# Kernel tuning notes

Measured on AMD Instinct MI355X. Metric: run time of the kernel, lower is better.

Reference implementation:

```python
import jax, jax.numpy as jnp
import numpy as np

N, D, B, K, H, E = 100000, 128, 4096, 64, 256, 128
DIN = D + 1
DELAYED_REWARD_STEP = 100.0


def setup_inputs() -> dict:
    key = jax.random.key(0)
    ks = jax.random.split(key, 16)
    s = 0.02
    d = {}
    d["node_pre_embedding"] = jax.random.normal(ks[0], (N, D), jnp.float32)
    d["steps"] = jax.random.uniform(ks[1], (B,), jnp.float32) * 50.0
    d["h0"] = jax.random.normal(ks[2], (B, H), jnp.float32) * 0.1
    d["c0"] = jax.random.normal(ks[3], (B, H), jnp.float32) * 0.1
    # MLP1: D_in -> 256 -> 128 (action embed, feeds LSTM input)
    d["W1a"] = jax.random.normal(ks[4], (256, DIN), jnp.float32) * s
    d["b1a"] = jnp.zeros((256,), jnp.float32)
    d["W1b"] = jax.random.normal(ks[5], (128, 256), jnp.float32) * s
    d["b1b"] = jnp.zeros((128,), jnp.float32)
    # MLP2: D_in -> 256 -> 128 (neighbor graph embed)
    d["W2a"] = jax.random.normal(ks[6], (256, DIN), jnp.float32) * s
    d["b2a"] = jnp.zeros((256,), jnp.float32)
    d["W2b"] = jax.random.normal(ks[7], (128, 256), jnp.float32) * s
    d["b2b"] = jnp.zeros((128,), jnp.float32)
    # MLP3: lstm_hidden (256) -> 128, single linear (hidden_dims3=[128])
    d["W3"] = jax.random.normal(ks[8], (E, H), jnp.float32) * s
    d["b3"] = jnp.zeros((E,), jnp.float32)
    # LSTMCell (PyTorch layout: gates i,f,g,o stacked on dim 0)
    d["Wih"] = jax.random.normal(ks[9], (4 * H, 128), jnp.float32) * s
    d["Whh"] = jax.random.normal(ks[10], (4 * H, H), jnp.float32) * s
    d["bih"] = jnp.zeros((4 * H,), jnp.float32)
    d["bhh"] = jnp.zeros((4 * H,), jnp.float32)
    # packed ragged adjacency: padded neighbor ids + per-row degree
    d["actions0"] = jax.random.randint(ks[11], (B,), 0, N)
    d["neighbors"] = jax.random.randint(ks[12], (B, K), 0, N)
    d["deg"] = jax.random.randint(ks[13], (B,), 1, K + 1)
    return d


def reference(node_pre_embedding, steps, h0, c0,
              W1a, b1a, W1b, b1b, W2a, b2a, W2b, b2b, W3, b3,
              Wih, Whh, bih, bhh, actions0, neighbors, deg):
    step_scaled = steps / DELAYED_REWARD_STEP  # [B]

    # --- graph embeddings for padded neighbors (ragged gather + MLP2) ---
    nei_feat = node_pre_embedding[neighbors]  # [B, K, D]
    step_col = jnp.broadcast_to(step_scaled[:, None, None], (B, K, 1))
    pre = jnp.concatenate([nei_feat, step_col], axis=-1)  # [B, K, D_in]
    g = jax.nn.relu(jnp.einsum('bkd,hd->bkh', pre, W2a) + b2a)
    g = jnp.einsum('bkh,eh->bke', g, W2b) + b2b  # [B, K, E]

    # --- action embedding: MLP1 -> LSTMCell -> MLP3 ---
    a_pre = jnp.concatenate([node_pre_embedding[actions0], step_scaled[:, None]], axis=-1)
    x = jax.nn.relu(a_pre @ W1a.T + b1a) @ W1b.T + b1b  # [B, 128]
    gates = x @ Wih.T + bih + h0 @ Whh.T + bhh  # [B, 4H]
    i, f, gg, o = jnp.split(gates, 4, axis=-1)
    c = jax.nn.sigmoid(f) * c0 + jax.nn.sigmoid(i) * jnp.tanh(gg)
    h = jax.nn.sigmoid(o) * jnp.tanh(c)
    emb = h @ W3.T + b3  # [B, E]

    # --- scaled dot-product scores, masked at padding ---
    vals = jnp.einsum('bke,be->bk', g, emb) / jnp.sqrt(jnp.float32(E))
    mask = jnp.arange(K)[None, :] < jnp.maximum(deg, 1)[:, None]
    vals = jnp.where(mask, vals, 0.0)
    return vals, h, c
```

## Files before the change

### kernel.cpp

```cpp
#include <hip/hip_runtime.h>
#include <hip/hip_bf16.h>

#define NN 100000
#define DD 128
#define BB 4096
#define KK 64
#define HH 256
#define EE 128

typedef __bf16 bf16x8 __attribute__((ext_vector_type(8)));
typedef float f32x4 __attribute__((ext_vector_type(4)));

#define EL_W1A 0
#define EL_W1B 32768
#define EL_WIH 65536
#define EL_WHH 196608
#define EL_W3  458752
#define EL_W2B 491520
#define EL_W2A 524288

#define BOFF_GB     0x110000
#define BOFF_W1COL  0x111000
#define BOFF_W2COL  0x111400
#define BOFF_CONST  0x111800
#define BOFF_T      0x115800

__device__ __forceinline__ float sigmoid_f(float x){ return 1.0f/(1.0f+__expf(-x)); }
__device__ __forceinline__ float tanh_f(float x){ return 1.0f - 2.0f/(__expf(2.0f*x)+1.0f); }

__device__ __forceinline__ bf16x8 pack8(float4 a, float4 b){
    bf16x8 v;
    v[0]=(__bf16)a.x; v[1]=(__bf16)a.y; v[2]=(__bf16)a.z; v[3]=(__bf16)a.w;
    v[4]=(__bf16)b.x; v[5]=(__bf16)b.y; v[6]=(__bf16)b.z; v[7]=(__bf16)b.w;
    return v;
}

__global__ __launch_bounds__(64) void swz_kernel(
    const float* __restrict__ W1a, const float* __restrict__ W1b,
    const float* __restrict__ Wih, const float* __restrict__ Whh,
    const float* __restrict__ W3,  const float* __restrict__ W2b,
    const float* __restrict__ W2a, const float* __restrict__ bih,
    const float* __restrict__ bhh, __bf16* __restrict__ wsbf,
    float* __restrict__ gb_ws, float* __restrict__ w1col_ws,
    float* __restrict__ w2col_ws)
{
    int g = blockIdx.x, lane = threadIdx.x;
    if (g >= 1088){
        if (g < 1104){ int idx = (g-1088)*64 + lane; gb_ws[idx] = bih[idx] + bhh[idx]; }
        else if (g < 1108){ int idx = (g-1104)*64 + lane; w1col_ws[idx] = W1a[idx*129 + 128]; }
        else { int idx = (g-1108)*64 + lane; w2col_ws[idx] = W2a[idx*129 + 128]; }
        return;
    }
    int quad = lane >> 4, l15 = lane & 15;
    const float* src; int stride, nkk, local; long dst; bool kn = false;
    if      (g <  64){ src=W1a; stride=129; nkk=4; dst=EL_W1A; local=g;      }
    else if (g < 128){ src=W1b; stride=256; nkk=8; dst=EL_W1B; local=g-64;   }
    else if (g < 384){ src=Wih; stride=128; nkk=4; dst=EL_WIH; local=g-128;  }
    else if (g < 896){ src=Whh; stride=256; nkk=8; dst=EL_WHH; local=g-384;  }
    else if (g < 960){ src=W3;  stride=256; nkk=8; dst=EL_W3;  local=g-896;  }
    else if (g <1024){ src=W2b; stride=256; nkk=4; dst=EL_W2B; local=g-960; kn=true; }
    else             { src=W2a; stride=129; nkk=4; dst=EL_W2A; local=g-1024; }
    int nt = local / nkk, kk = local % nkk;
    int n = nt*16 + l15, k0 = kk*32 + quad*8;
    bf16x8 v;
#pragma unroll
    for (int j = 0; j < 8; ++j){
        float x = kn ? src[(long)(k0+j)*stride + n] : src[(long)n*stride + k0 + j];
        v[j] = (__bf16)x;
    }
    ((bf16x8*)(wsbf + dst))[local*64 + lane] = v;
}

__global__ __launch_bounds__(256) void act_kernel(
    const float* __restrict__ node_pre, const float* __restrict__ steps,
    const float* __restrict__ h0, const float* __restrict__ c0_in,
    const float* __restrict__ b1a, const float* __restrict__ b1b,
    const float* __restrict__ b3, const float* __restrict__ b2b,
    const int* __restrict__ actions0, const float* __restrict__ gb_ws,
    const float* __restrict__ w1col, const __bf16* __restrict__ wsbf,
    float* __restrict__ out_h, float* __restrict__ out_c,
    __bf16* __restrict__ t_bf, float* __restrict__ const_ws)
{
    __shared__ __bf16 apre[16*136];
    __shared__ __bf16 x1s [16*264];
    __shared__ __bf16 h0s [16*264];
    __shared__ float b1a_s[256], w1c_s[256], b1b_s[128], gbs[1024];
    __shared__ float b3_s[128], b2b_s[128], sb_s[16];

    int tid = threadIdx.x, b0 = blockIdx.x * 16;
    b1a_s[tid] = b1a[tid];
    w1c_s[tid] = w1col[tid];
    if (tid < 128){ b1b_s[tid] = b1b[tid]; b3_s[tid] = b3[tid]; b2b_s[tid] = b2b[tid]; }
    for (int ch = tid; ch < 1024; ch += 256) gbs[ch] = gb_ws[ch];
    if (tid < 16) sb_s[tid] = steps[b0 + tid] * 0.01f;
    {
        int r = tid >> 4, seg = tid & 15;
        long a0 = actions0[b0 + r];
        const float4* sp = (const float4*)(node_pre + a0*128 + seg*8);
        float4 f0 = sp[0], f1 = sp[1];
        *(bf16x8*)&apre[r*136 + seg*8] = pack8(f0, f1);
    }
    for (int ch = tid; ch < 512; ch += 256){
        int r = ch >> 5, sg = ch & 31;
        const float4* sp = (const float4*)(h0 + (long)(b0+r)*256 + sg*8);
        float4 a = sp[0], b = sp[1];
        *(bf16x8*)&h0s[r*264 + sg*8] = pack8(a, b);
    }
    __syncthreads();

    int wave = tid >> 6, lane = tid & 63, quad = lane >> 4, l15 = lane & 15;
    const bf16x8* F1A = (const bf16x8*)(wsbf + EL_W1A);
    const bf16x8* F1B = (const bf16x8*)(wsbf + EL_W1B);
    const bf16x8* FIH = (const bf16x8*)(wsbf + EL_WIH);
    const bf16x8* FHH = (const bf16x8*)(wsbf + EL_WHH);
    const bf16x8* F3  = (const bf16x8*)(wsbf + EL_W3);
    const bf16x8* F2B = (const bf16x8*)(wsbf + EL_W2B);

    {
        bf16x8 af[4];
#pragma unroll
        for (int kk = 0; kk < 4; ++kk)
            af[kk] = *(const bf16x8*)&apre[l15*136 + kk*32 + quad*8];
#pragma unroll
        for (int j = 0; j < 4; ++j){
            int nt = wave*4 + j;
            f32x4 acc = {0.f,0.f,0.f,0.f};
#pragma unroll
            for (int kk = 0; kk < 4; ++kk)
                acc = __builtin_amdgcn_mfma_f32_16x16x32_bf16(af[kk], F1A[(nt*4+kk)*64 + lane], acc, 0,0,0);
            int col = nt*16 + l15;
            float bb = b1a_s[col], wc = w1c_s[col];
#pragma unroll
            for (int i = 0; i < 4; ++i){
                int r = quad*4 + i;
                x1s[r*264 + col] = (__bf16)fmaxf(acc[i] + bb + wc*sb_s[r], 0.f);
            }
        }
    }
    __syncthreads();

    {
        bf16x8 af[8];
#pragma unroll
        for (int kk = 0; kk < 8; ++kk)
            af[kk] = *(const bf16x8*)&x1s[l15*264 + kk*32 + quad*8];
#pragma unroll
        for (int j = 0; j < 2; ++j){
            int nt = wave*2 + j;
            f32x4 acc = {0.f,0.f,0.f,0.f};
#pragma unroll
            for (int kk = 0; kk < 8; ++kk)
                acc = __builtin_amdgcn_mfma_f32_16x16x32_bf16(af[kk], F1B[(nt*8+kk)*64 + lane], acc, 0,0,0);
            int col = nt*16 + l15;
#pragma unroll
            for (int i = 0; i < 4; ++i)
                apre[(quad*4+i)*136 + col] = (__bf16)(acc[i] + b1b_s[col]);
        }
    }
    __syncthreads();

    {
        bf16x8 af[12];
#pragma unroll
        for (int kk = 0; kk < 4; ++kk)
            af[kk] = *(const bf16x8*)&apre[l15*136 + kk*32 + quad*8];
#pragma unroll
        for (int kk = 0; kk < 8; ++kk)
            af[4+kk] = *(const bf16x8*)&h0s[l15*264 + kk*32 + quad*8];

#pragma unroll 1
        for (int jj = 0; jj < 4; ++jj){
            int ct = wave*4 + jj;
            f32x4 aI = {0.f,0.f,0.f,0.f}, aF = aI, aG = aI, aO = aI;
#pragma unroll
            for (int kk = 0; kk < 4; ++kk){
                aI = __builtin_amdgcn_mfma_f32_16x16x32_bf16(af[kk], FIH[(( 0+ct)*4+kk)*64 + lane], aI, 0,0,0);
                aF = __builtin_amdgcn_mfma_f32_16x16x32_bf16(af[kk], FIH[((16+ct)*4+kk)*64 + lane], aF, 0,0,0);
                aG = __builtin_amdgcn_mfma_f32_16x16x32_bf16(af[kk], FIH[((32+ct)*4+kk)*64 + lane], aG, 0,0,0);
                aO = __builtin_amdgcn_mfma_f32_16x16x32_bf16(af[kk], FIH[((48+ct)*4+kk)*64 + lane], aO, 0,0,0);
            }
#pragma unroll 4
            for (int k2 = 0; k2 < 8; ++k2){
                aI = __builtin_amdgcn_mfma_f32_16x16x32_bf16(af[4+k2], FHH[(( 0+ct)*8+k2)*64 + lane], aI, 0,0,0);
                aF = __builtin_amdgcn_mfma_f32_16x16x32_bf16(af[4+k2], FHH[((16+ct)*8+k2)*64 + lane], aF, 0,0,0);
                aG = __builtin_amdgcn_mfma_f32_16x16x32_bf16(af[4+k2], FHH[((32+ct)*8+k2)*64 + lane], aG, 0,0,0);
                aO = __builtin_amdgcn_mfma_f32_16x16x32_bf16(af[4+k2], FHH[((48+ct)*8+k2)*64 + lane], aO, 0,0,0);
            }
            int col = ct*16 + l15;
            float bI = gbs[col], bF = gbs[256+col], bG = gbs[512+col], bO = gbs[768+col];
#pragma unroll
            for (int i = 0; i < 4; ++i){
                long row = b0 + quad*4 + i;
                float iv = aI[i]+bI, fv = aF[i]+bF, gv = aG[i]+bG, ov = aO[i]+bO;
                float cc = c0_in[row*256 + col];
                float cn = sigmoid_f(fv)*cc + sigmoid_f(iv)*tanh_f(gv);
                float hn = sigmoid_f(ov)*tanh_f(cn);
                out_c[row*256 + col] = cn;
                out_h[row*256 + col] = hn;
                x1s[(quad*4+i)*264 + col] = (__bf16)hn;
            }
        }
    }
    __syncthreads();

    {
        bf16x8 af[8];
#pragma unroll
        for (int kk = 0; kk < 8; ++kk)
            af[kk] = *(const bf16x8*)&x1s[l15*264 + kk*32 + quad*8];
#pragma unroll
        for (int j = 0; j < 2; ++j){
            int nt = wave*2 + j;
            f32x4 acc = {0.f,0.f,0.f,0.f};
#pragma unroll
            for (int kk = 0; kk < 8; ++kk)
                acc = __builtin_amdgcn_mfma_f32_16x16x32_bf16(af[kk], F3[(nt*8+kk)*64 + lane], acc, 0,0,0);
            int col = nt*16 + l15;
#pragma unroll
            for (int i = 0; i < 4; ++i)
                apre[(quad*4+i)*136 + col] = (__bf16)(acc[i] + b3_s[col]);
        }
    }
    __syncthreads();

    {
        int r = tid >> 4, p = tid & 15;
        float s = 0.f;
#pragma unroll
        for (int q = 0; q < 8; ++q) s += b2b_s[p*8+q] * (float)apre[r*136 + p*8 + q];
#pragma unroll
        for (int m = 1; m < 16; m <<= 1) s += __shfl_xor(s, m, 64);
        if (p == 0) const_ws[b0 + r] = s;
    }
    {
        bf16x8 ef[4];
#pragma unroll
        for (int kk = 0; kk < 4; ++kk)
            ef[kk] = *(const bf16x8*)&apre[l15*136 + kk*32 + quad*8];
#pragma unroll
        for (int j = 0; j < 4; ++j){
            int nt = wave*4 + j;
            f32x4 acc = {0.f,0.f,0.f,0.f};
#pragma unroll
            for (int kk = 0; kk < 4; ++kk)
                acc = __builtin_amdgcn_mfma_f32_16x16x32_bf16(ef[kk], F2B[(nt*4+kk)*64 + lane], acc, 0,0,0);
            int col = nt*16 + l15;
#pragma unroll
            for (int i = 0; i < 4; ++i)
                t_bf[(long)(b0 + quad*4 + i)*256 + col] = (__bf16)acc[i];
        }
    }
}

__global__ __launch_bounds__(256) void nei_kernel(
    const float* __restrict__ node_pre, const float* __restrict__ steps,
    const float* __restrict__ b2a, const float* __restrict__ w2col,
    const int* __restrict__ neighbors, const int* __restrict__ deg,
    const __bf16* __restrict__ wsbf, const __bf16* __restrict__ t_bf,
    const float* __restrict__ const_ws, float* __restrict__ out_vals)
{
    __shared__ __bf16 at[64*136];
    __shared__ float t_s[256], b2a_s[256], w2c_s[256], vp[256];

    int tid = threadIdx.x, blk = blockIdx.x;
    b2a_s[tid] = b2a[tid];
    w2c_s[tid] = w2col[tid];

    int wave = tid >> 6, lane = tid & 63, quad = lane >> 4, l15 = lane & 15;
    const bf16x8* FB = (const bf16x8*)(wsbf + EL_W2A);
    bf16x8 bw[16];
#pragma unroll
    for (int j = 0; j < 4; ++j){
        int nt = wave + 4*j;
#pragma unroll
        for (int kk = 0; kk < 4; ++kk) bw[j*4+kk] = FB[(nt*4+kk)*64 + lane];
    }

#pragma unroll 1
    for (int ib = 0; ib < 4; ++ib){
        int b = blk*4 + ib;
        __syncthreads();
        int degb = deg[b]; if (degb < 1) degb = 1;
        int ntile = (degb + 15) >> 4;
        t_s[tid] = (float)t_bf[(long)b*256 + tid];
        {
            int r = tid >> 2, sg = tid & 3;
            if (r < ntile*16){
                long nb = neighbors[b*64 + r];
                const float4* sp = (const float4*)(node_pre + nb*128 + sg*32);
#pragma unroll
                for (int q = 0; q < 4; ++q){
                    float4 fa = sp[q*2], fb = sp[q*2+1];
                    *(bf16x8*)&at[r*136 + sg*32 + q*8] = pack8(fa, fb);
                }
            }
        }
        __syncthreads();

        float sb = steps[b] * 0.01f;
#pragma unroll 1
        for (int mt = 0; mt < ntile; ++mt){
            bf16x8 af[4];
#pragma unroll
            for (int kk = 0; kk < 4; ++kk)
                af[kk] = *(const bf16x8*)&at[(mt*16 + l15)*136 + kk*32 + quad*8];
            f32x4 ps = {0.f,0.f,0.f,0.f};
#pragma unroll
            for (int j = 0; j < 4; ++j){
                int nt = wave + 4*j;
                f32x4 acc = {0.f,0.f,0.f,0.f};
#pragma unroll
                for (int kk = 0; kk < 4; ++kk)
                    acc = __builtin_amdgcn_mfma_f32_16x16x32_bf16(af[kk], bw[j*4+kk], acc, 0,0,0);
                int col = nt*16 + l15;
                float bb = b2a_s[col] + w2c_s[col]*sb;
                float tv = t_s[col];
#pragma unroll
                for (int i = 0; i < 4; ++i)
                    ps[i] += fmaxf(acc[i] + bb, 0.f) * tv;
            }
#pragma unroll
            for (int m = 1; m < 16; m <<= 1){
#pragma unroll
                for (int i = 0; i < 4; ++i) ps[i] += __shfl_xor(ps[i], m, 64);
            }
            if (l15 == 0){
#pragma unroll
                for (int i = 0; i < 4; ++i) vp[wave*64 + mt*16 + quad*4 + i] = ps[i];
            }
        }
        __syncthreads();
        if (tid < 64){
            float v = vp[tid] + vp[64+tid] + vp[128+tid] + vp[192+tid];
            v = (v + const_ws[b]) * 0.08838834764831845f;
            if (tid >= degb) v = 0.f;
            out_vals[(long)b*64 + tid] = v;
        }
    }
}

extern "C" void kernel_launch(void* const* d_in, const int* in_sizes, int n_in,
                              void* d_out, int out_size, void* d_ws, size_t ws_size,
                              hipStream_t stream)
{
    (void)in_sizes; (void)n_in; (void)out_size; (void)ws_size;
    const float* node_pre = (const float*)d_in[0];
    const float* steps    = (const float*)d_in[1];
    const float* h0       = (const float*)d_in[2];
    const float* c0       = (const float*)d_in[3];
    const float* W1a      = (const float*)d_in[4];
    const float* b1a      = (const float*)d_in[5];
    const float* W1b      = (const float*)d_in[6];
    const float* b1b      = (const float*)d_in[7];
    const float* W2a      = (const float*)d_in[8];
    const float* b2a      = (const float*)d_in[9];
    const float* W2b      = (const float*)d_in[10];
    const float* b2b      = (const float*)d_in[11];
    const float* W3       = (const float*)d_in[12];
    const float* b3       = (const float*)d_in[13];
    const float* Wih      = (const float*)d_in[14];
    const float* Whh      = (const float*)d_in[15];
    const float* bih      = (const float*)d_in[16];
    const float* bhh      = (const float*)d_in[17];
    const int* actions0   = (const int*)d_in[18];
    const int* neighbors  = (const int*)d_in[19];
    const int* deg        = (const int*)d_in[20];

    float* out      = (float*)d_out;
    float* out_vals = out;
    float* out_h    = out + (long)BB*KK;
    float* out_c    = out_h + (long)BB*HH;

    __bf16* wsbf     = (__bf16*)d_ws;
    float* gb_ws     = (float*)((char*)d_ws + BOFF_GB);
    float* w1col_ws  = (float*)((char*)d_ws + BOFF_W1COL);
    float* w2col_ws  = (float*)((char*)d_ws + BOFF_W2COL);
    float* const_ws  = (float*)((char*)d_ws + BOFF_CONST);
    __bf16* t_bf     = (__bf16*)((char*)d_ws + BOFF_T);

    swz_kernel<<<dim3(1112), dim3(64), 0, stream>>>(W1a, W1b, Wih, Whh, W3, W2b, W2a,
                                                    bih, bhh, wsbf, gb_ws, w1col_ws, w2col_ws);
    act_kernel<<<dim3(256), dim3(256), 0, stream>>>(node_pre, steps, h0, c0, b1a, b1b, b3, b2b,
                                                    actions0, gb_ws, w1col_ws, wsbf,
                                                    out_h, out_c, t_bf, const_ws);
    nei_kernel<<<dim3(1024), dim3(256), 0, stream>>>(node_pre, steps, b2a, w2col_ws,
                                                     neighbors, deg, wsbf, t_bf, const_ws,
                                                     out_vals);
}
```

Baseline: 221.4 us.

## Split action pipeline into per-stage kernels and give each neighbor row its own block

After: 181.4 us. 1.22x faster.

```diff
diff --git a/kernel.cpp b/kernel.cpp
--- a/kernel.cpp
+++ b/kernel.cpp
@@ -23,7 +23,12 @@
 #define BOFF_W1COL  0x111000
 #define BOFF_W2COL  0x111400
 #define BOFF_CONST  0x111800
-#define BOFF_T      0x115800
+#define BOFF_X1     0x115800
+#define BOFF_X      0x315800
+#define BOFF_H0B    0x415800
+#define BOFF_HB     0x615800
+#define BOFF_EMB    0x815800
+#define BOFF_T      0x915800
 
 __device__ __forceinline__ float sigmoid_f(float x){ return 1.0f/(1.0f+__expf(-x)); }
 __device__ __forceinline__ float tanh_f(float x){ return 1.0f - 2.0f/(__expf(2.0f*x)+1.0f); }
@@ -40,15 +45,21 @@
     const float* __restrict__ Wih, const float* __restrict__ Whh,
     const float* __restrict__ W3,  const float* __restrict__ W2b,
     const float* __restrict__ W2a, const float* __restrict__ bih,
-    const float* __restrict__ bhh, __bf16* __restrict__ wsbf,
-    float* __restrict__ gb_ws, float* __restrict__ w1col_ws,
-    float* __restrict__ w2col_ws)
+    const float* __restrict__ bhh, const float* __restrict__ h0,
+    __bf16* __restrict__ wsbf, float* __restrict__ gb_ws,
+    float* __restrict__ w1col_ws, float* __restrict__ w2col_ws,
+    __bf16* __restrict__ h0_bf)
 {
     int g = blockIdx.x, lane = threadIdx.x;
     if (g >= 1088){
         if (g < 1104){ int idx = (g-1088)*64 + lane; gb_ws[idx] = bih[idx] + bhh[idx]; }
         else if (g < 1108){ int idx = (g-1104)*64 + lane; w1col_ws[idx] = W1a[idx*129 + 128]; }
-        else { int idx = (g-1108)*64 + lane; w2col_ws[idx] = W2a[idx*129 + 128]; }
+        else if (g < 1112){ int idx = (g-1108)*64 + lane; w2col_ws[idx] = W2a[idx*129 + 128]; }
+        else {
+            long i = (long)(g-1112)*64 + lane;
+            const float4* sp = (const float4*)h0 + i*2;
+            ((bf16x8*)h0_bf)[i] = pack8(sp[0], sp[1]);
+        }
         return;
     }
     int quad = lane >> 4, l15 = lane & 15;
@@ -71,184 +82,174 @@
     ((bf16x8*)(wsbf + dst))[local*64 + lane] = v;
 }
 
-__global__ __launch_bounds__(256) void act_kernel(
+__global__ __launch_bounds__(64) void s1_kernel(
     const float* __restrict__ node_pre, const float* __restrict__ steps,
-    const float* __restrict__ h0, const float* __restrict__ c0_in,
-    const float* __restrict__ b1a, const float* __restrict__ b1b,
-    const float* __restrict__ b3, const float* __restrict__ b2b,
-    const int* __restrict__ actions0, const float* __restrict__ gb_ws,
+    const int* __restrict__ actions0, const float* __restrict__ b1a,
     const float* __restrict__ w1col, const __bf16* __restrict__ wsbf,
-    float* __restrict__ out_h, float* __restrict__ out_c,
-    __bf16* __restrict__ t_bf, float* __restrict__ const_ws)
-{
-    __shared__ __bf16 apre[16*136];
-    __shared__ __bf16 x1s [16*264];
-    __shared__ __bf16 h0s [16*264];
-    __shared__ float b1a_s[256], w1c_s[256], b1b_s[128], gbs[1024];
-    __shared__ float b3_s[128], b2b_s[128], sb_s[16];
-
-    int tid = threadIdx.x, b0 = blockIdx.x * 16;
-    b1a_s[tid] = b1a[tid];
-    w1c_s[tid] = w1col[tid];
-    if (tid < 128){ b1b_s[tid] = b1b[tid]; b3_s[tid] = b3[tid]; b2b_s[tid] = b2b[tid]; }
-    for (int ch = tid; ch < 1024; ch += 256) gbs[ch] = gb_ws[ch];
-    if (tid < 16) sb_s[tid] = steps[b0 + tid] * 0.01f;
-    {
-        int r = tid >> 4, seg = tid & 15;
-        long a0 = actions0[b0 + r];
-        const float4* sp = (const float4*)(node_pre + a0*128 + seg*8);
-        float4 f0 = sp[0], f1 = sp[1];
-        *(bf16x8*)&apre[r*136 + seg*8] = pack8(f0, f1);
-    }
-    for (int ch = tid; ch < 512; ch += 256){
-        int r = ch >> 5, sg = ch & 31;
-        const float4* sp = (const float4*)(h0 + (long)(b0+r)*256 + sg*8);
-        float4 a = sp[0], b = sp[1];
-        *(bf16x8*)&h0s[r*264 + sg*8] = pack8(a, b);
-    }
-    __syncthreads();
-
-    int wave = tid >> 6, lane = tid & 63, quad = lane >> 4, l15 = lane & 15;
-    const bf16x8* F1A = (const bf16x8*)(wsbf + EL_W1A);
-    const bf16x8* F1B = (const bf16x8*)(wsbf + EL_W1B);
+    __bf16* __restrict__ x1_bf)
+{
+    int lane = threadIdx.x, quad = lane >> 4, l15 = lane & 15;
+    int mt = blockIdx.x >> 2, ng = blockIdx.x & 3, m0 = mt*16;
+    long arow = actions0[m0 + l15];
+    bf16x8 af[4];
+#pragma unroll
+    for (int kk = 0; kk < 4; ++kk){
+        const float4* p = (const float4*)(node_pre + arow*128 + kk*32 + quad*8);
+        af[kk] = pack8(p[0], p[1]);
+    }
+    float sb_i[4];
+#pragma unroll
+    for (int i = 0; i < 4; ++i) sb_i[i] = steps[m0 + quad*4 + i] * 0.01f;
+    const bf16x8* FB = (const bf16x8*)(wsbf + EL_W1A);
+#pragma unroll
+    for (int j = 0; j < 4; ++j){
+        int nt = ng*4 + j;
+        f32x4 acc = {0.f,0.f,0.f,0.f};
+#pragma unroll
+        for (int kk = 0; kk < 4; ++kk)
+            acc = __builtin_amdgcn_mfma_f32_16x16x32_bf16(af[kk], FB[(nt*4+kk)*64 + lane], acc, 0,0,0);
+        int col = nt*16 + l15;
+        float bb = b1a[col], wc = w1col[col];
+#pragma unroll
+        for (int i = 0; i < 4; ++i)
+            x1_bf[(long)(m0 + quad*4 + i)*256 + col] = (__bf16)fmaxf(acc[i] + bb + wc*sb_i[i], 0.f);
+    }
+}
+
+__global__ __launch_bounds__(64) void s2_kernel(
+    const __bf16* __restrict__ x1_bf, const float* __restrict__ b1b,
+    const __bf16* __restrict__ wsbf, __bf16* __restrict__ x_bf)
+{
+    int lane = threadIdx.x, quad = lane >> 4, l15 = lane & 15;
+    int mt = blockIdx.x >> 2, ng = blockIdx.x & 3, m0 = mt*16;
+    bf16x8 af[8];
+#pragma unroll
+    for (int kk = 0; kk < 8; ++kk)
+        af[kk] = *(const bf16x8*)&x1_bf[(long)(m0 + l15)*256 + kk*32 + quad*8];
+    const bf16x8* FB = (const bf16x8*)(wsbf + EL_W1B);
+#pragma unroll
+    for (int j = 0; j < 2; ++j){
+        int nt = ng*2 + j;
+        f32x4 acc = {0.f,0.f,0.f,0.f};
+#pragma unroll
+        for (int kk = 0; kk < 8; ++kk)
+            acc = __builtin_amdgcn_mfma_f32_16x16x32_bf16(af[kk], FB[(nt*8+kk)*64 + lane], acc, 0,0,0);
+        int col = nt*16 + l15;
+        float bb = b1b[col];
+#pragma unroll
+        for (int i = 0; i < 4; ++i)
+            x_bf[(long)(m0 + quad*4 + i)*128 + col] = (__bf16)(acc[i] + bb);
+    }
+}
+
+__global__ __launch_bounds__(64) void lstm_kernel(
+    const __bf16* __restrict__ x_bf, const __bf16* __restrict__ h0_bf,
+    const float* __restrict__ c0_in, const float* __restrict__ gb_ws,
+    const __bf16* __restrict__ wsbf,
+    float* __restrict__ out_h, float* __restrict__ out_c, __bf16* __restrict__ h_bf)
+{
+    int lane = threadIdx.x, quad = lane >> 4, l15 = lane & 15;
+    int mt = blockIdx.x >> 4, ct = blockIdx.x & 15, m0 = mt*16;
+    bf16x8 af[12];
+#pragma unroll
+    for (int kk = 0; kk < 4; ++kk)
+        af[kk] = *(const bf16x8*)&x_bf[(long)(m0 + l15)*128 + kk*32 + quad*8];
+#pragma unroll
+    for (int kk = 0; kk < 8; ++kk)
+        af[4+kk] = *(const bf16x8*)&h0_bf[(long)(m0 + l15)*256 + kk*32 + quad*8];
+
     const bf16x8* FIH = (const bf16x8*)(wsbf + EL_WIH);
     const bf16x8* FHH = (const bf16x8*)(wsbf + EL_WHH);
-    const bf16x8* F3  = (const bf16x8*)(wsbf + EL_W3);
-    const bf16x8* F2B = (const bf16x8*)(wsbf + EL_W2B);
-
-    {
-        bf16x8 af[4];
+    f32x4 aI = {0.f,0.f,0.f,0.f}, aF = aI, aG = aI, aO = aI;
+#pragma unroll
+    for (int kk = 0; kk < 4; ++kk){
+        aI = __builtin_amdgcn_mfma_f32_16x16x32_bf16(af[kk], FIH[(( 0+ct)*4+kk)*64 + lane], aI, 0,0,0);
+        aF = __builtin_amdgcn_mfma_f32_16x16x32_bf16(af[kk], FIH[((16+ct)*4+kk)*64 + lane], aF, 0,0,0);
+        aG = __builtin_amdgcn_mfma_f32_16x16x32_bf16(af[kk], FIH[((32+ct)*4+kk)*64 + lane], aG, 0,0,0);
+        aO = __builtin_amdgcn_mfma_f32_16x16x32_bf16(af[kk], FIH[((48+ct)*4+kk)*64 + lane], aO, 0,0,0);
+    }
+#pragma unroll
+    for (int k2 = 0; k2 < 8; ++k2){
+        aI = __builtin_amdgcn_mfma_f32_16x16x32_bf16(af[4+k2], FHH[(( 0+ct)*8+k2)*64 + lane], aI, 0,0,0);
+        aF = __builtin_amdgcn_mfma_f32_16x16x32_bf16(af[4+k2], FHH[((16+ct)*8+k2)*64 + lane], aF, 0,0,0);
+        aG = __builtin_amdgcn_mfma_f32_16x16x32_bf16(af[4+k2], FHH[((32+ct)*8+k2)*64 + lane], aG, 0,0,0);
+        aO = __builtin_amdgcn_mfma_f32_16x16x32_bf16(af[4+k2], FHH[((48+ct)*8+k2)*64 + lane], aO, 0,0,0);
+    }
+    int col = ct*16 + l15;
+    float bI = gb_ws[col], bF = gb_ws[256+col], bG = gb_ws[512+col], bO = gb_ws[768+col];
+#pragma unroll
+    for (int i = 0; i < 4; ++i){
+        long row = m0 + quad*4 + i;
+        float iv = aI[i]+bI, fv = aF[i]+bF, gv = aG[i]+bG, ov = aO[i]+bO;
+        float cc = c0_in[row*256 + col];
+        float cn = sigmoid_f(fv)*cc + sigmoid_f(iv)*tanh_f(gv);
+        float hn = sigmoid_f(ov)*tanh_f(cn);
+        out_c[row*256 + col] = cn;
+        out_h[row*256 + col] = hn;
+        h_bf[row*256 + col] = (__bf16)hn;
+    }
+}
+
+__global__ __launch_bounds__(64) void s4_kernel(
+    const __bf16* __restrict__ h_bf, const float* __restrict__ b3,
+    const __bf16* __restrict__ wsbf, __bf16* __restrict__ emb_bf)
+{
+    int lane = threadIdx.x, quad = lane >> 4, l15 = lane & 15;
+    int mt = blockIdx.x >> 2, ng = blockIdx.x & 3, m0 = mt*16;
+    bf16x8 af[8];
+#pragma unroll
+    for (int kk = 0; kk < 8; ++kk)
+        af[kk] = *(const bf16x8*)&h_bf[(long)(m0 + l15)*256 + kk*32 + quad*8];
+    const bf16x8* FB = (const bf16x8*)(wsbf + EL_W3);
+#pragma unroll
+    for (int j = 0; j < 2; ++j){
+        int nt = ng*2 + j;
+        f32x4 acc = {0.f,0.f,0.f,0.f};
+#pragma unroll
+        for (int kk = 0; kk < 8; ++kk)
+            acc = __builtin_amdgcn_mfma_f32_16x16x32_bf16(af[kk], FB[(nt*8+kk)*64 + lane], acc, 0,0,0);
+        int col = nt*16 + l15;
+        float bb = b3[col];
+#pragma unroll
+        for (int i = 0; i < 4; ++i)
+            emb_bf[(long)(m0 + quad*4 + i)*128 + col] = (__bf16)(acc[i] + bb);
+    }
+}
+
+__global__ __launch_bounds__(64) void s5_kernel(
+    const __bf16* __restrict__ emb_bf, const float* __restrict__ b2b,
+    const __bf16* __restrict__ wsbf, __bf16* __restrict__ t_bf,
+    float* __restrict__ const_ws)
+{
+    int lane = threadIdx.x, quad = lane >> 4, l15 = lane & 15;
+    int mt = blockIdx.x >> 2, ng = blockIdx.x & 3, m0 = mt*16;
+    bf16x8 af[4];
+#pragma unroll
+    for (int kk = 0; kk < 4; ++kk)
+        af[kk] = *(const bf16x8*)&emb_bf[(long)(m0 + l15)*128 + kk*32 + quad*8];
+    if (ng == 0){
+        float s = 0.f;
 #pragma unroll
         for (int kk = 0; kk < 4; ++kk)
-            af[kk] = *(const bf16x8*)&apre[l15*136 + kk*32 + quad*8];
-#pragma unroll
-        for (int j = 0; j < 4; ++j){
-            int nt = wave*4 + j;
-            f32x4 acc = {0.f,0.f,0.f,0.f};
-#pragma unroll
-            for (int kk = 0; kk < 4; ++kk)
-                acc = __builtin_amdgcn_mfma_f32_16x16x32_bf16(af[kk], F1A[(nt*4+kk)*64 + lane], acc, 0,0,0);
-            int col = nt*16 + l15;
-            float bb = b1a_s[col], wc = w1c_s[col];
-#pragma unroll
-            for (int i = 0; i < 4; ++i){
-                int r = quad*4 + i;
-                x1s[r*264 + col] = (__bf16)fmaxf(acc[i] + bb + wc*sb_s[r], 0.f);
-            }
-        }
-    }
-    __syncthreads();
-
-    {
-        bf16x8 af[8];
-#pragma unroll
-        for (int kk = 0; kk < 8; ++kk)
-            af[kk] = *(const bf16x8*)&x1s[l15*264 + kk*32 + quad*8];
-#pragma unroll
-        for (int j = 0; j < 2; ++j){
-            int nt = wave*2 + j;
-            f32x4 acc = {0.f,0.f,0.f,0.f};
-#pragma unroll
-            for (int kk = 0; kk < 8; ++kk)
-                acc = __builtin_amdgcn_mfma_f32_16x16x32_bf16(af[kk], F1B[(nt*8+kk)*64 + lane], acc, 0,0,0);
-            int col = nt*16 + l15;
-#pragma unroll
-            for (int i = 0; i < 4; ++i)
-                apre[(quad*4+i)*136 + col] = (__bf16)(acc[i] + b1b_s[col]);
-        }
-    }
-    __syncthreads();
-
-    {
-        bf16x8 af[12];
+#pragma unroll
+            for (int j = 0; j < 8; ++j)
+                s += b2b[kk*32 + quad*8 + j] * (float)af[kk][j];
+        s += __shfl_xor(s, 16, 64);
+        s += __shfl_xor(s, 32, 64);
+        if (lane < 16) const_ws[m0 + l15] = s;
+    }
+    const bf16x8* FB = (const bf16x8*)(wsbf + EL_W2B);
+#pragma unroll
+    for (int j = 0; j < 4; ++j){
+        int nt = ng*4 + j;
+        f32x4 acc = {0.f,0.f,0.f,0.f};
 #pragma unroll
         for (int kk = 0; kk < 4; ++kk)
-            af[kk] = *(const bf16x8*)&apre[l15*136 + kk*32 + quad*8];
-#pragma unroll
-        for (int kk = 0; kk < 8; ++kk)
-            af[4+kk] = *(const bf16x8*)&h0s[l15*264 + kk*32 + quad*8];
-
-#pragma unroll 1
-        for (int jj = 0; jj < 4; ++jj){
-            int ct = wave*4 + jj;
-            f32x4 aI = {0.f,0.f,0.f,0.f}, aF = aI, aG = aI, aO = aI;
-#pragma unroll
-            for (int kk = 0; kk < 4; ++kk){
-                aI = __builtin_amdgcn_mfma_f32_16x16x32_bf16(af[kk], FIH[(( 0+ct)*4+kk)*64 + lane], aI, 0,0,0);
-                aF = __builtin_amdgcn_mfma_f32_16x16x32_bf16(af[kk], FIH[((16+ct)*4+kk)*64 + lane], aF, 0,0,0);
-                aG = __builtin_amdgcn_mfma_f32_16x16x32_bf16(af[kk], FIH[((32+ct)*4+kk)*64 + lane], aG, 0,0,0);
-                aO = __builtin_amdgcn_mfma_f32_16x16x32_bf16(af[kk], FIH[((48+ct)*4+kk)*64 + lane], aO, 0,0,0);
-            }
-#pragma unroll 4
-            for (int k2 = 0; k2 < 8; ++k2){
-                aI = __builtin_amdgcn_mfma_f32_16x16x32_bf16(af[4+k2], FHH[(( 0+ct)*8+k2)*64 + lane], aI, 0,0,0);
-                aF = __builtin_amdgcn_mfma_f32_16x16x32_bf16(af[4+k2], FHH[((16+ct)*8+k2)*64 + lane], aF, 0,0,0);
-                aG = __builtin_amdgcn_mfma_f32_16x16x32_bf16(af[4+k2], FHH[((32+ct)*8+k2)*64 + lane], aG, 0,0,0);
-                aO = __builtin_amdgcn_mfma_f32_16x16x32_bf16(af[4+k2], FHH[((48+ct)*8+k2)*64 + lane], aO, 0,0,0);
-            }
-            int col = ct*16 + l15;
-            float bI = gbs[col], bF = gbs[256+col], bG = gbs[512+col], bO = gbs[768+col];
-#pragma unroll
-            for (int i = 0; i < 4; ++i){
-                long row = b0 + quad*4 + i;
-                float iv = aI[i]+bI, fv = aF[i]+bF, gv = aG[i]+bG, ov = aO[i]+bO;
-                float cc = c0_in[row*256 + col];
-                float cn = sigmoid_f(fv)*cc + sigmoid_f(iv)*tanh_f(gv);
-                float hn = sigmoid_f(ov)*tanh_f(cn);
-                out_c[row*256 + col] = cn;
-                out_h[row*256 + col] = hn;
-                x1s[(quad*4+i)*264 + col] = (__bf16)hn;
-            }
-        }
-    }
-    __syncthreads();
-
-    {
-        bf16x8 af[8];
-#pragma unroll
-        for (int kk = 0; kk < 8; ++kk)
-            af[kk] = *(const bf16x8*)&x1s[l15*264 + kk*32 + quad*8];
-#pragma unroll
-        for (int j = 0; j < 2; ++j){
-            int nt = wave*2 + j;
-            f32x4 acc = {0.f,0.f,0.f,0.f};
-#pragma unroll
-            for (int kk = 0; kk < 8; ++kk)
-                acc = __builtin_amdgcn_mfma_f32_16x16x32_bf16(af[kk], F3[(nt*8+kk)*64 + lane], acc, 0,0,0);
-            int col = nt*16 + l15;
-#pragma unroll
-            for (int i = 0; i < 4; ++i)
-                apre[(quad*4+i)*136 + col] = (__bf16)(acc[i] + b3_s[col]);
-        }
-    }
-    __syncthreads();
-
-    {
-        int r = tid >> 4, p = tid & 15;
-        float s = 0.f;
-#pragma unroll
-        for (int q = 0; q < 8; ++q) s += b2b_s[p*8+q] * (float)apre[r*136 + p*8 + q];
-#pragma unroll
-        for (int m = 1; m < 16; m <<= 1) s += __shfl_xor(s, m, 64);
-        if (p == 0) const_ws[b0 + r] = s;
-    }
-    {
-        bf16x8 ef[4];
-#pragma unroll
-        for (int kk = 0; kk < 4; ++kk)
-            ef[kk] = *(const bf16x8*)&apre[l15*136 + kk*32 + quad*8];
-#pragma unroll
-        for (int j = 0; j < 4; ++j){
-            int nt = wave*4 + j;
-            f32x4 acc = {0.f,0.f,0.f,0.f};
-#pragma unroll
-            for (int kk = 0; kk < 4; ++kk)
-                acc = __builtin_amdgcn_mfma_f32_16x16x32_bf16(ef[kk], F2B[(nt*4+kk)*64 + lane], acc, 0,0,0);
-            int col = nt*16 + l15;
-#pragma unroll
-            for (int i = 0; i < 4; ++i)
-                t_bf[(long)(b0 + quad*4 + i)*256 + col] = (__bf16)acc[i];
-        }
+            acc = __builtin_amdgcn_mfma_f32_16x16x32_bf16(af[kk], FB[(nt*4+kk)*64 + lane], acc, 0,0,0);
+        int col = nt*16 + l15;
+#pragma unroll
+        for (int i = 0; i < 4; ++i)
+            t_bf[(long)(m0 + quad*4 + i)*256 + col] = (__bf16)acc[i];
     }
 }
 
@@ -260,11 +261,26 @@
     const float* __restrict__ const_ws, float* __restrict__ out_vals)
 {
     __shared__ __bf16 at[64*136];
-    __shared__ float t_s[256], b2a_s[256], w2c_s[256], vp[256];
-
-    int tid = threadIdx.x, blk = blockIdx.x;
-    b2a_s[tid] = b2a[tid];
-    w2c_s[tid] = w2col[tid];
+    __shared__ float t_s[256], bias_s[256], vp[256];
+
+    int tid = threadIdx.x, b = blockIdx.x;
+    int degb = deg[b]; if (degb < 1) degb = 1;
+    int ntile = (degb + 15) >> 4;
+    float sb = steps[b] * 0.01f;
+    t_s[tid]    = (float)t_bf[(long)b*256 + tid];
+    bias_s[tid] = b2a[tid] + w2col[tid]*sb;
+    {
+        int r = tid >> 2, sg = tid & 3;
+        if (r < ntile*16){
+            long nb = neighbors[b*64 + r];
+            const float4* sp = (const float4*)(node_pre + nb*128 + sg*32);
+#pragma unroll
+            for (int q = 0; q < 4; ++q){
+                float4 fa = sp[q*2], fb = sp[q*2+1];
+                *(bf16x8*)&at[r*136 + sg*32 + q*8] = pack8(fa, fb);
+            }
+        }
+    }
 
     int wave = tid >> 6, lane = tid & 63, quad = lane >> 4, l15 = lane & 15;
     const bf16x8* FB = (const bf16x8*)(wsbf + EL_W2A);
@@ -275,67 +291,44 @@
 #pragma unroll
         for (int kk = 0; kk < 4; ++kk) bw[j*4+kk] = FB[(nt*4+kk)*64 + lane];
     }
+    __syncthreads();
 
 #pragma unroll 1
-    for (int ib = 0; ib < 4; ++ib){
-        int b = blk*4 + ib;
-        __syncthreads();
-        int degb = deg[b]; if (degb < 1) degb = 1;
-        int ntile = (degb + 15) >> 4;
-        t_s[tid] = (float)t_bf[(long)b*256 + tid];
-        {
-            int r = tid >> 2, sg = tid & 3;
-            if (r < ntile*16){
-                long nb = neighbors[b*64 + r];
-                const float4* sp = (const float4*)(node_pre + nb*128 + sg*32);
-#pragma unroll
-                for (int q = 0; q < 4; ++q){
-                    float4 fa = sp[q*2], fb = sp[q*2+1];
-                    *(bf16x8*)&at[r*136 + sg*32 + q*8] = pack8(fa, fb);
-                }
-            }
-        }
-        __syncthreads();
-
-        float sb = steps[b] * 0.01f;
-#pragma unroll 1
-        for (int mt = 0; mt < ntile; ++mt){
-            bf16x8 af[4];
+    for (int mt = 0; mt < ntile; ++mt){
+        bf16x8 af[4];
+#pragma unroll
+        for (int kk = 0; kk < 4; ++kk)
+            af[kk] = *(const bf16x8*)&at[(mt*16 + l15)*136 + kk*32 + quad*8];
+        f32x4 ps = {0.f,0.f,0.f,0.f};
+#pragma unroll
+        for (int j = 0; j < 4; ++j){
+            int nt = wave + 4*j;
+            f32x4 acc = {0.f,0.f,0.f,0.f};
 #pragma unroll
             for (int kk = 0; kk < 4; ++kk)
-                af[kk] = *(const bf16x8*)&at[(mt*16 + l15)*136 + kk*32 + quad*8];
-            f32x4 ps = {0.f,0.f,0.f,0.f};
-#pragma unroll
-            for (int j = 0; j < 4; ++j){
-                int nt = wave + 4*j;
-                f32x4 acc = {0.f,0.f,0.f,0.f};
-#pragma unroll
-                for (int kk = 0; kk < 4; ++kk)
-                    acc = __builtin_amdgcn_mfma_f32_16x16x32_bf16(af[kk], bw[j*4+kk], acc, 0,0,0);
-                int col = nt*16 + l15;
-                float bb = b2a_s[col] + w2c_s[col]*sb;
-                float tv = t_s[col];
-#pragma unroll
-                for (int i = 0; i < 4; ++i)
-                    ps[i] += fmaxf(acc[i] + bb, 0.f) * tv;
-            }
-#pragma unroll
-            for (int m = 1; m < 16; m <<= 1){
-#pragma unroll
-                for (int i = 0; i < 4; ++i) ps[i] += __shfl_xor(ps[i], m, 64);
-            }
-            if (l15 == 0){
-#pragma unroll
-                for (int i = 0; i < 4; ++i) vp[wave*64 + mt*16 + quad*4 + i] = ps[i];
-            }
-        }
-        __syncthreads();
-        if (tid < 64){
-            float v = vp[tid] + vp[64+tid] + vp[128+tid] + vp[192+tid];
-            v = (v + const_ws[b]) * 0.08838834764831845f;
-            if (tid >= degb) v = 0.f;
-            out_vals[(long)b*64 + tid] = v;
-        }
+                acc = __builtin_amdgcn_mfma_f32_16x16x32_bf16(af[kk], bw[j*4+kk], acc, 0,0,0);
+            int col = nt*16 + l15;
+            float bb = bias_s[col], tv = t_s[col];
+#pragma unroll
+            for (int i = 0; i < 4; ++i)
+                ps[i] += fmaxf(acc[i] + bb, 0.f) * tv;
+        }
+#pragma unroll
+        for (int m = 1; m < 16; m <<= 1){
+#pragma unroll
+            for (int i = 0; i < 4; ++i) ps[i] += __shfl_xor(ps[i], m, 64);
+        }
+        if (l15 == 0){
+#pragma unroll
+            for (int i = 0; i < 4; ++i) vp[wave*64 + mt*16 + quad*4 + i] = ps[i];
+        }
+    }
+    __syncthreads();
+    if (tid < 64){
+        float v = vp[tid] + vp[64+tid] + vp[128+tid] + vp[192+tid];
+        v = (v + const_ws[b]) * 0.08838834764831845f;
+        if (tid >= degb) v = 0.f;
+        out_vals[(long)b*64 + tid] = v;
     }
 }
 
@@ -376,14 +369,24 @@
     float* w1col_ws  = (float*)((char*)d_ws + BOFF_W1COL);
     float* w2col_ws  = (float*)((char*)d_ws + BOFF_W2COL);
     float* const_ws  = (float*)((char*)d_ws + BOFF_CONST);
+    __bf16* x1_bf    = (__bf16*)((char*)d_ws + BOFF_X1);
+    __bf16* x_bf     = (__bf16*)((char*)d_ws + BOFF_X);
+    __bf16* h0_bf    = (__bf16*)((char*)d_ws + BOFF_H0B);
+    __bf16* h_bf     = (__bf16*)((char*)d_ws + BOFF_HB);
+    __bf16* emb_bf   = (__bf16*)((char*)d_ws + BOFF_EMB);
     __bf16* t_bf     = (__bf16*)((char*)d_ws + BOFF_T);
 
-    swz_kernel<<<dim3(1112), dim3(64), 0, stream>>>(W1a, W1b, Wih, Whh, W3, W2b, W2a,
-                                                    bih, bhh, wsbf, gb_ws, w1col_ws, w2col_ws);
-    act_kernel<<<dim3(256), dim3(256), 0, stream>>>(node_pre, steps, h0, c0, b1a, b1b, b3, b2b,
-                                                    actions0, gb_ws, w1col_ws, wsbf,
-                                                    out_h, out_c, t_bf, const_ws);
-    nei_kernel<<<dim3(1024), dim3(256), 0, stream>>>(node_pre, steps, b2a, w2col_ws,
+    swz_kernel<<<dim3(3160), dim3(64), 0, stream>>>(W1a, W1b, Wih, Whh, W3, W2b, W2a,
+                                                    bih, bhh, h0, wsbf, gb_ws,
+                                                    w1col_ws, w2col_ws, h0_bf);
+    s1_kernel<<<dim3(1024), dim3(64), 0, stream>>>(node_pre, steps, actions0, b1a,
+                                                   w1col_ws, wsbf, x1_bf);
+    s2_kernel<<<dim3(1024), dim3(64), 0, stream>>>(x1_bf, b1b, wsbf, x_bf);
+    lstm_kernel<<<dim3(4096), dim3(64), 0, stream>>>(x_bf, h0_bf, c0, gb_ws, wsbf,
+                                                     out_h, out_c, h_bf);
+    s4_kernel<<<dim3(1024), dim3(64), 0, stream>>>(h_bf, b3, wsbf, emb_bf);
+    s5_kernel<<<dim3(1024), dim3(64), 0, stream>>>(emb_bf, b2b, wsbf, t_bf, const_ws);
+    nei_kernel<<<dim3(4096), dim3(256), 0, stream>>>(node_pre, steps, b2a, w2col_ws,
                                                      neighbors, deg, wsbf, t_bf, const_ws,
                                                      out_vals);
 }
```
